# Kernel tuning notes

Measured on AMD Instinct MI355X. Metric: run time of the kernel, lower is better.

## Reference

```python
import jax, jax.numpy as jnp
import numpy as np

KERNEL = 3
STRIDE = 1
PADDING = 1


def _extract_patches(x, k, stride, padding, h_out, w_out):
    # x: [B, C, H, W] -> patches [k, k, B, C, h_out, w_out]
    if padding > 0:
        x = jnp.pad(x, ((0, 0), (0, 0), (padding, padding), (padding, padding)))
    rows = []
    for di in range(k):
        cols = []
        for dj in range(k):
            sl = x[:, :, di:di + (h_out - 1) * stride + 1:stride,
                        dj:dj + (w_out - 1) * stride + 1:stride]
            cols.append(sl)
        rows.append(jnp.stack(cols, axis=0))
    return jnp.stack(rows, axis=0)  # [k, k, B, C, h_out, w_out]


def setup_inputs() -> dict:
    key = jax.random.key(0)
    k1, k2 = jax.random.split(key)
    B, C_in, C_out, H, W = 32, 64, 64, 32, 32
    h_out = (H + 2 * PADDING - KERNEL) // STRIDE + 1
    w_out = (W + 2 * PADDING - KERNEL) // STRIDE + 1
    fan_in = C_in * KERNEL ** 2
    x = jax.random.normal(k1, (B, C_in, H, W), dtype=jnp.float32)
    weight = jax.random.normal(
        k2, (h_out, w_out, C_out, C_in, KERNEL, KERNEL), dtype=jnp.float32
    ) / np.sqrt(fan_in).astype(np.float32)
    bias = jnp.zeros((C_out, h_out, w_out), dtype=jnp.float32)
    return {"x": x, "weight": weight, "bias": bias}


def reference(x, weight, bias):
    h_out, w_out = weight.shape[0], weight.shape[1]
    # patches: [k, k, B, C, h_out, w_out]
    patches = _extract_patches(x, KERNEL, STRIDE, PADDING, h_out, w_out)
    # unshared-weight contraction per spatial location
    # weight: [h_out(x), w_out(y), O, C(i), k(k), k(l)]
    out = jnp.einsum('xyoikl,klbixy->boxy', weight, patches)
    return out + bias[None, :, :, :]
```

## Files before the change

kernel.cpp:

```cpp
#include <hip/hip_runtime.h>

#define HH 32
#define WW 32
#define CIN 64
#define COUT 64
#define BATCH 32
#define KTOT 576
#define NPOS 1024
#define KC 8
#define KHALF 288
#define NCW 36

__device__ float g_xT[CIN * 34 * 34 * BATCH];

__global__ __launch_bounds__(256) void repack_kernel(const float* __restrict__ x) {
    __shared__ float tile[32 * 33];
    const int i   = blockIdx.x;
    const int hh  = blockIdx.y;
    const int tid = threadIdx.x;

    float* dst = &g_xT[((i * 34 + hh) * 34) * BATCH];

    if (hh == 0 || hh == 33) {
        for (int idx = tid; idx < 34 * BATCH; idx += 256) dst[idx] = 0.f;
        return;
    }
    const int hs = hh - 1;
#pragma unroll
    for (int bb = 0; bb < 4; ++bb) {
        int b = bb * 8 + (tid >> 5);
        int w = tid & 31;
        tile[b * 33 + w] = x[(b << 16) + (i << 10) + (hs << 5) + w];
    }
    __syncthreads();
#pragma unroll
    for (int q = 0; q < 5; ++q) {
        int ww = q * 8 + (tid >> 5);
        if (ww < 34) {
            int b = tid & 31;
            float v = (ww == 0 || ww == 33) ? 0.f : tile[b * 33 + (ww - 1)];
            dst[ww * BATCH + b] = v;
        }
    }
}

__device__ __forceinline__ void async16(const void* src, void* dst_lds) {
    __builtin_amdgcn_global_load_lds(
        (const __attribute__((address_space(1))) void*)src,
        (__attribute__((address_space(3))) void*)dst_lds,
        16, 0, 0);
}

__global__ __launch_bounds__(128, 2) void local2d_kernel(
    const float* __restrict__ weight,
    const float* __restrict__ bias,
    float* __restrict__ out)
{
    __shared__ float Wl[2][3][32 * KC];
    __shared__ float Pl[2][3][KC * BATCH];

    const int wv = threadIdx.x >> 6;
    const int l  = threadIdx.x & 63;

    const int og = l & 7, bg = l >> 3;

    int bid = blockIdx.x;
    int xcd = bid & 7;
    int t   = bid >> 3;
    int oh  = t & 1;
    int tt  = t >> 1;
    int y   = ((tt >> 5) << 3) | xcd;
    int xw  = tt & 31;
    int p   = (y << 5) | xw;

    const int kbase = wv * KHALF;
    const float* wpos = weight + ((long)p * COUT + (oh << 5)) * KTOT;
    const float* wsrc0 =
        wpos + (((l & 7) << 2) + (l >> 4)) * KTOT + (((l >> 3) & 1) << 2) + kbase;

    float acc[4][4];
#pragma unroll
    for (int a = 0; a < 4; ++a)
#pragma unroll
        for (int c = 0; c < 4; ++c) acc[a][c] = 0.f;

    auto stage = [&](int c, int bsel) {
        async16(wsrc0 + c * KC, &Wl[wv][bsel][0]);
        {
            int k  = kbase + c * KC + (l >> 3);
            int i  = k / 9;
            int r  = k - i * 9;
            int kh = r / 3;
            int kw = r - kh * 3;
            const float* ps =
                &g_xT[(((i * 34) + y + kh) * 34 + xw + kw) * BATCH + ((l & 7) << 2)];
            async16(ps, &Pl[wv][bsel][0]);
        }
    };

    auto compute = [&](int bsel) {
        const float* Wb = &Wl[wv][bsel][og << 2];
        const float* Pb = &Pl[wv][bsel][bg << 2];
#pragma unroll
        for (int kk = 0; kk < KC; kk += 4) {
            float4 pr[4];
#pragma unroll
            for (int j = 0; j < 4; ++j)
                pr[j] = *(const float4*)(Pb + (kk + j) * BATCH);
            const float* prf = (const float*)pr;
#pragma unroll
            for (int oo = 0; oo < 4; ++oo) {
                float4 wr = *(const float4*)(Wb + (oo << 6) + (kk << 3));
#pragma unroll
                for (int bb = 0; bb < 4; ++bb) {
                    float a = acc[oo][bb];
                    a = fmaf(wr.x, prf[0 * 4 + bb], a);
                    a = fmaf(wr.y, prf[1 * 4 + bb], a);
                    a = fmaf(wr.z, prf[2 * 4 + bb], a);
                    a = fmaf(wr.w, prf[3 * 4 + bb], a);
                    acc[oo][bb] = a;
                }
            }
        }
    };

    stage(0, 0);
    stage(1, 1);
    for (int c = 0; c < NCW - 1; ++c) {
        asm volatile("s_waitcnt vmcnt(2)" ::: "memory");
        asm volatile("s_waitcnt lgkmcnt(0)" ::: "memory");
        if (c + 2 < NCW) stage(c + 2, (c + 2) % 3);
        compute(c % 3);
    }
    asm volatile("s_waitcnt vmcnt(0)" ::: "memory");
    compute((NCW - 1) % 3);

    __syncthreads();
    float* R = &Wl[0][0][0];
    if (wv == 1) {
#pragma unroll
        for (int oo = 0; oo < 4; ++oo) {
            int o = (og << 2) + oo;
            *(float4*)(&R[o * 36 + (bg << 2)]) =
                make_float4(acc[oo][0], acc[oo][1], acc[oo][2], acc[oo][3]);
        }
    }
    __syncthreads();
    if (wv == 0) {
#pragma unroll
        for (int oo = 0; oo < 4; ++oo) {
            int o  = (og << 2) + oo;
            int of = (oh << 5) + o;
            float bv = bias[(of << 10) + p];
            float4 r = *(const float4*)(&R[o * 36 + (bg << 2)]);
            const float* rf = (const float*)&r;
#pragma unroll
            for (int bb = 0; bb < 4; ++bb) {
                int b = (bg << 2) + bb;
                out[(b << 16) + (of << 10) + p] = acc[oo][bb] + rf[bb] + bv;
            }
        }
    }
}

extern "C" void kernel_launch(void* const* d_in, const int* in_sizes, int n_in,
                              void* d_out, int out_size, void* d_ws, size_t ws_size,
                              hipStream_t stream) {
    const float* x      = (const float*)d_in[0];
    const float* weight = (const float*)d_in[1];
    const float* bias   = (const float*)d_in[2];
    float* out          = (float*)d_out;

    hipLaunchKernelGGL(repack_kernel, dim3(CIN, 34), dim3(256), 0, stream, x);
    hipLaunchKernelGGL(local2d_kernel, dim3(2 * NPOS), dim3(128), 0, stream,
                       weight, bias, out);
}
```

Measured before the change: 252.9 us.

## Split K across eight waves with whole weight tile staged in LDS

The main kernel moves from 128 to 512 threads per block. It loads the block's full 32x576 weight slice into LDS once with plain float4 loads and splits the K reduction across eight waves instead of two. Patch values are now read straight from global memory into registers rather than through async LDS staging. The goal is more waves in flight and higher memory-level parallelism for this bandwidth-bound, weight-streaming workload. In exchange it drops the triple-buffered async pipeline, uses about 72KB of LDS per block, and adds an eight-way LDS reduction at the end.

```diff
diff --git a/kernel.cpp b/kernel.cpp
--- a/kernel.cpp
+++ b/kernel.cpp
@@ -1,15 +1,10 @@
 #include <hip/hip_runtime.h>
 
-#define HH 32
-#define WW 32
 #define CIN 64
 #define COUT 64
 #define BATCH 32
 #define KTOT 576
 #define NPOS 1024
-#define KC 8
-#define KHALF 288
-#define NCW 36
 
 __device__ float g_xT[CIN * 34 * 34 * BATCH];
 
@@ -44,25 +39,18 @@
     }
 }
 
-__device__ __forceinline__ void async16(const void* src, void* dst_lds) {
-    __builtin_amdgcn_global_load_lds(
-        (const __attribute__((address_space(1))) void*)src,
-        (__attribute__((address_space(3))) void*)dst_lds,
-        16, 0, 0);
-}
-
-__global__ __launch_bounds__(128, 2) void local2d_kernel(
+__global__ __launch_bounds__(512, 4) void local2d_kernel(
     const float* __restrict__ weight,
     const float* __restrict__ bias,
     float* __restrict__ out)
 {
-    __shared__ float Wl[2][3][32 * KC];
-    __shared__ float Pl[2][3][KC * BATCH];
+    __shared__ __align__(16) float lds[144 * 32 * 4];
 
-    const int wv = threadIdx.x >> 6;
-    const int l  = threadIdx.x & 63;
-
-    const int og = l & 7, bg = l >> 3;
+    const int tid = threadIdx.x;
+    const int wv  = tid >> 6;
+    const int l   = tid & 63;
+    const int bg  = l & 7;
+    const int og2 = l >> 3;
 
     int bid = blockIdx.x;
     int xcd = bid & 7;
@@ -73,10 +61,16 @@
     int xw  = tt & 31;
     int p   = (y << 5) | xw;
 
-    const int kbase = wv * KHALF;
-    const float* wpos = weight + ((long)p * COUT + (oh << 5)) * KTOT;
-    const float* wsrc0 =
-        wpos + (((l & 7) << 2) + (l >> 4)) * KTOT + (((l >> 3) & 1) << 2) + kbase;
+    {
+        const float* src = weight + ((long)p * COUT + (oh << 5)) * KTOT
+                         + (tid & 31) * KTOT + ((tid >> 5) << 2);
+#pragma unroll
+        for (int q = 0; q < 9; ++q) {
+            *(float4*)(&lds[((q << 9) + tid) << 2]) =
+                *(const float4*)(src + (q << 6));
+        }
+    }
+    __syncthreads();
 
     float acc[4][4];
 #pragma unroll
@@ -84,81 +78,65 @@
 #pragma unroll
         for (int c = 0; c < 4; ++c) acc[a][c] = 0.f;
 
-    auto stage = [&](int c, int bsel) {
-        async16(wsrc0 + c * KC, &Wl[wv][bsel][0]);
-        {
-            int k  = kbase + c * KC + (l >> 3);
-            int i  = k / 9;
-            int r  = k - i * 9;
-            int kh = r / 3;
-            int kw = r - kh * 3;
-            const float* ps =
-                &g_xT[(((i * 34) + y + kh) * 34 + xw + kw) * BATCH + ((l & 7) << 2)];
-            async16(ps, &Pl[wv][bsel][0]);
+    const float* pb = g_xT + (((wv << 3) * 1156 + y * 34 + xw) << 5) + (bg << 2);
+    const float* wb = &lds[(wv * 2304) + (og2 << 2)];
+
+#pragma unroll
+    for (int g = 0; g < 18; ++g) {
+        float4 pr[4];
+#pragma unroll
+        for (int j = 0; j < 4; ++j) {
+            const int c  = 4 * g + j;
+            const int di = c / 9;
+            const int rr = c - 9 * di;
+            const int kh = rr / 3;
+            const int kw = rr - 3 * kh;
+            pr[j] = *(const float4*)(pb + ((di * 1156 + kh * 34 + kw) << 5));
         }
-    };
-
-    auto compute = [&](int bsel) {
-        const float* Wb = &Wl[wv][bsel][og << 2];
-        const float* Pb = &Pl[wv][bsel][bg << 2];
+        const float* prf = (const float*)pr;
 #pragma unroll
-        for (int kk = 0; kk < KC; kk += 4) {
-            float4 pr[4];
+        for (int oc = 0; oc < 4; ++oc) {
+            float4 wr = *(const float4*)(wb + (g << 7) + (oc << 5));
 #pragma unroll
-            for (int j = 0; j < 4; ++j)
-                pr[j] = *(const float4*)(Pb + (kk + j) * BATCH);
-            const float* prf = (const float*)pr;
-#pragma unroll
-            for (int oo = 0; oo < 4; ++oo) {
-                float4 wr = *(const float4*)(Wb + (oo << 6) + (kk << 3));
-#pragma unroll
-                for (int bb = 0; bb < 4; ++bb) {
-                    float a = acc[oo][bb];
-                    a = fmaf(wr.x, prf[0 * 4 + bb], a);
-                    a = fmaf(wr.y, prf[1 * 4 + bb], a);
-                    a = fmaf(wr.z, prf[2 * 4 + bb], a);
-                    a = fmaf(wr.w, prf[3 * 4 + bb], a);
-                    acc[oo][bb] = a;
-                }
+            for (int bb = 0; bb < 4; ++bb) {
+                float a = acc[oc][bb];
+                a = fmaf(wr.x, prf[0 * 4 + bb], a);
+                a = fmaf(wr.y, prf[1 * 4 + bb], a);
+                a = fmaf(wr.z, prf[2 * 4 + bb], a);
+                a = fmaf(wr.w, prf[3 * 4 + bb], a);
+                acc[oc][bb] = a;
             }
         }
-    };
-
-    stage(0, 0);
-    stage(1, 1);
-    for (int c = 0; c < NCW - 1; ++c) {
-        asm volatile("s_waitcnt vmcnt(2)" ::: "memory");
-        asm volatile("s_waitcnt lgkmcnt(0)" ::: "memory");
-        if (c + 2 < NCW) stage(c + 2, (c + 2) % 3);
-        compute(c % 3);
     }
-    asm volatile("s_waitcnt vmcnt(0)" ::: "memory");
-    compute((NCW - 1) % 3);
 
     __syncthreads();
-    float* R = &Wl[0][0][0];
-    if (wv == 1) {
+    if (wv != 0) {
+        float* R = &lds[(wv - 1) * 1152];
 #pragma unroll
-        for (int oo = 0; oo < 4; ++oo) {
-            int o = (og << 2) + oo;
+        for (int oc = 0; oc < 4; ++oc) {
+            int o = (oc << 3) + og2;
             *(float4*)(&R[o * 36 + (bg << 2)]) =
-                make_float4(acc[oo][0], acc[oo][1], acc[oo][2], acc[oo][3]);
+                make_float4(acc[oc][0], acc[oc][1], acc[oc][2], acc[oc][3]);
         }
     }
     __syncthreads();
     if (wv == 0) {
 #pragma unroll
-        for (int oo = 0; oo < 4; ++oo) {
-            int o  = (og << 2) + oo;
+        for (int oc = 0; oc < 4; ++oc) {
+            int o  = (oc << 3) + og2;
             int of = (oh << 5) + o;
+            float s0 = acc[oc][0], s1 = acc[oc][1], s2 = acc[oc][2], s3 = acc[oc][3];
+#pragma unroll
+            for (int s = 0; s < 7; ++s) {
+                float4 r = *(const float4*)(&lds[s * 1152 + o * 36 + (bg << 2)]);
+                s0 += r.x; s1 += r.y; s2 += r.z; s3 += r.w;
+            }
             float bv = bias[(of << 10) + p];
-            float4 r = *(const float4*)(&R[o * 36 + (bg << 2)]);
-            const float* rf = (const float*)&r;
-#pragma unroll
-            for (int bb = 0; bb < 4; ++bb) {
-                int b = (bg << 2) + bb;
-                out[(b << 16) + (of << 10) + p] = acc[oo][bb] + rf[bb] + bv;
-            }
+            int b0 = bg << 2;
+            out[((b0 + 0) << 16) + (of << 10) + p] = s0 + bv;
+            out[((b0 + 1) << 16) + (of << 10) + p] = s1 + bv;
+            out[((b0 + 2) << 16) + (of << 10) + p] = s2 + bv;
+            out[((b0 + 3) << 16) + (of << 10) + p] = s3 + bv;
         }
     }
 }
@@ -172,6 +150,6 @@
     float* out          = (float*)d_out;
 
     hipLaunchKernelGGL(repack_kernel, dim3(CIN, 34), dim3(256), 0, stream, x);
-    hipLaunchKernelGGL(local2d_kernel, dim3(2 * NPOS), dim3(128), 0, stream,
+    hipLaunchKernelGGL(local2d_kernel, dim3(2 * NPOS), dim3(512), 0, stream,
                        weight, bias, out);
 }
```

After: 262.7 us. +3.9%, slower.
